# Performance work log

Measured on AMD Instinct MI355X. Metric: run time of the kernel, lower is better.

## Reference

```python
import jax, jax.numpy as jnp
import numpy as np

C = 4096
IN_DIM = 256
OUT_DIM = 64
H = 4
NEG_SLOPE = 0.2


def setup_inputs() -> dict:
    key = jax.random.key(0)
    k_x, k_adj, k_w, k_as, k_ad = jax.random.split(key, 5)
    x = jax.random.normal(k_x, (C, IN_DIM), dtype=jnp.float32)
    adj = jax.random.randint(k_adj, (C, C), 0, 2, dtype=jnp.int32)
    # xavier_uniform for Linear(in, out*H): bound = sqrt(6/(fan_in+fan_out))
    bw = float(np.sqrt(6.0 / (IN_DIM + OUT_DIM * H)))
    W = jax.random.uniform(k_w, (IN_DIM, OUT_DIM * H), minval=-bw, maxval=bw, dtype=jnp.float32)
    ba = float(np.sqrt(6.0 / (H + OUT_DIM)))
    a_src = jax.random.uniform(k_as, (H, OUT_DIM), minval=-ba, maxval=ba, dtype=jnp.float32)
    a_dst = jax.random.uniform(k_ad, (H, OUT_DIM), minval=-ba, maxval=ba, dtype=jnp.float32)
    return {"x": x, "adj": adj, "W": W, "a_src": a_src, "a_dst": a_dst}


def reference(x, adj, W, a_src, a_dst):
    # h: [C, H, D] -> h_heads: [H, C, D]
    h = (x @ W).reshape(C, H, OUT_DIM)
    h_heads = jnp.transpose(h, (1, 0, 2))
    # per-node additive attention logits: [H, C]
    alpha_src = jnp.einsum('hcd,hd->hc', h_heads, a_src)
    alpha_dst = jnp.einsum('hcd,hd->hc', h_heads, a_dst)
    # broadcast scores e: [H, C, C]
    e = alpha_src[:, :, None] + alpha_dst[:, None, :]
    e = jnp.where(e >= 0, e, NEG_SLOPE * e)  # LeakyReLU
    e = jnp.where(adj[None, :, :] == 0, -jnp.inf, e)
    attn = jax.nn.softmax(e, axis=-1)  # [H, C, C]
    out = jnp.einsum('hcj,hjd->hcd', attn, h_heads)  # [H, C, D]
    return jnp.transpose(out, (1, 0, 2)).reshape(C, H * OUT_DIM)
```

## Files before the change

kernel.cpp:

```cpp
#include <hip/hip_runtime.h>
#include <math.h>

#define CN 4096
#define KDIM 256
#define ND 256
#define NH 4
#define DD 64
#define NEG 0.2f
#define L2E 1.44269504f

typedef __attribute__((ext_vector_type(8))) short short8;
typedef __attribute__((ext_vector_type(4))) float floatx4;

union S8I4 { int i[4]; short8 s; };

__device__ inline unsigned bfbits_rne(float f) {
  unsigned u = __float_as_uint(f);
  u += 0x7fffu + ((u >> 16) & 1u);
  return u >> 16;
}
__device__ inline float bf2f(unsigned hi) { return __uint_as_float(hi << 16); }

__device__ inline int pack2_trunc(float a, float b) {
  return (int)__builtin_amdgcn_perm(__float_as_uint(b), __float_as_uint(a), 0x07060302u);
}

#define GLDS(gp, lp, sz)                                                        \
  __builtin_amdgcn_global_load_lds(                                             \
      (const __attribute__((address_space(1))) void*)(gp),                      \
      (__attribute__((address_space(3))) void*)(lp), (sz), 0, 0)

__global__ __launch_bounds__(256) void k_wcvt(const float* __restrict__ W,
                                              unsigned short* __restrict__ WT_hi,
                                              unsigned short* __restrict__ WT_lo) {
  const int t = threadIdx.x;
  const int c = blockIdx.x * 4 + (t >> 6);
  const int k0 = (t & 63) * 4;
  unsigned h[4], l[4];
#pragma unroll
  for (int j = 0; j < 4; ++j) {
    const float w = W[(size_t)(k0 + j) * ND + c];
    h[j] = bfbits_rne(w);
    l[j] = bfbits_rne(w - bf2f(h[j]));
  }
  uint2 vh, vl;
  vh.x = h[0] | (h[1] << 16); vh.y = h[2] | (h[3] << 16);
  vl.x = l[0] | (l[1] << 16); vl.y = l[2] | (l[3] << 16);
  *(uint2*)&WT_hi[(size_t)c * KDIM + k0] = vh;
  *(uint2*)&WT_lo[(size_t)c * KDIM + k0] = vl;
}

__global__ __launch_bounds__(256) void k_pre(const int* __restrict__ adj,
                                             unsigned char* __restrict__ mbits8,
                                             const float* __restrict__ x,
                                             const unsigned short* __restrict__ WT_hi,
                                             const unsigned short* __restrict__ WT_lo,
                                             const float* __restrict__ a_src,
                                             const float* __restrict__ a_dst,
                                             unsigned short* __restrict__ hT,
                                             float2* __restrict__ Erow,
                                             float2* __restrict__ Ecol) {
  const int bx = blockIdx.x;
  const int t = threadIdx.x;
  if (bx >= 256) {
    const int w = t >> 6, lane = t & 63;
    const int row = (bx - 256) * 4 + w;
    const int4* __restrict__ src = (const int4*)(adj + (size_t)row * CN);
    unsigned char* __restrict__ dst = mbits8 + (size_t)row * 512;
#pragma unroll
    for (int it = 0; it < 8; ++it) {
      const int4 v0 = src[it * 128 + lane * 2];
      const int4 v1 = src[it * 128 + lane * 2 + 1];
      const unsigned b = (unsigned)(v0.x != 0)        | ((unsigned)(v0.y != 0) << 1) |
                         ((unsigned)(v0.z != 0) << 2) | ((unsigned)(v0.w != 0) << 3) |
                         ((unsigned)(v1.x != 0) << 4) | ((unsigned)(v1.y != 0) << 5) |
                         ((unsigned)(v1.z != 0) << 6) | ((unsigned)(v1.w != 0) << 7);
      dst[it * 64 + lane] = (unsigned char)b;
    }
    return;
  }
  const int lane = t & 63, ww = t >> 6;
  const int n = lane & 15, q = lane >> 4;
  const int head = bx >> 6;
  const int c0 = head * DD;
  const int i0 = (bx & 63) * 64 + ww * 16;
  const float* xr = x + (size_t)(i0 + n) * KDIM + q * 8;
  floatx4 acc[4] = {};
#pragma unroll 2
  for (int k0 = 0; k0 < KDIM; k0 += 32) {
    const float4 xa = *(const float4*)(xr + k0);
    const float4 xb = *(const float4*)(xr + k0 + 4);
    const float xs[8] = {xa.x, xa.y, xa.z, xa.w, xb.x, xb.y, xb.z, xb.w};
    S8I4 Ah, Al;
#pragma unroll
    for (int e = 0; e < 4; ++e) {
      const unsigned h0 = bfbits_rne(xs[2 * e]), h1 = bfbits_rne(xs[2 * e + 1]);
      const float r0 = xs[2 * e] - bf2f(h0), r1 = xs[2 * e + 1] - bf2f(h1);
      Ah.i[e] = (int)(h0 | (h1 << 16));
      Al.i[e] = (int)(bfbits_rne(r0) | (bfbits_rne(r1) << 16));
    }
#pragma unroll
    for (int tt = 0; tt < 4; ++tt) {
      const size_t boff = (size_t)(c0 + tt * 16 + n) * KDIM + k0 + q * 8;
      const short8 Bh = *(const short8*)(WT_hi + boff);
      const short8 Bl = *(const short8*)(WT_lo + boff);
      acc[tt] = __builtin_amdgcn_mfma_f32_16x16x32_bf16(Ah.s, Bh, acc[tt], 0, 0, 0);
      acc[tt] = __builtin_amdgcn_mfma_f32_16x16x32_bf16(Al.s, Bh, acc[tt], 0, 0, 0);
      acc[tt] = __builtin_amdgcn_mfma_f32_16x16x32_bf16(Ah.s, Bl, acc[tt], 0, 0, 0);
    }
  }
  unsigned short* hTb = hT + (size_t)head * DD * CN;
#pragma unroll
  for (int tt = 0; tt < 4; ++tt)
#pragma unroll
    for (int r = 0; r < 4; r += 2) {
      const unsigned d = bfbits_rne(acc[tt][r]) | (bfbits_rne(acc[tt][r + 1]) << 16);
      *(unsigned*)(hTb + (size_t)(tt * 16 + n) * CN + i0 + q * 4 + r) = d;
    }
  float ps[4] = {}, pd[4] = {};
#pragma unroll
  for (int tt = 0; tt < 4; ++tt) {
    const float as = a_src[head * DD + tt * 16 + n];
    const float ad = a_dst[head * DD + tt * 16 + n];
#pragma unroll
    for (int r = 0; r < 4; ++r) {
      ps[r] += acc[tt][r] * as;
      pd[r] += acc[tt][r] * ad;
    }
  }
#pragma unroll
  for (int off = 1; off < 16; off <<= 1)
#pragma unroll
    for (int r = 0; r < 4; ++r) {
      ps[r] += __shfl_xor(ps[r], off);
      pd[r] += __shfl_xor(pd[r], off);
    }
  if (n == 0) {
#pragma unroll
    for (int r = 0; r < 4; ++r) {
      const int i = i0 + q * 4 + r;
      const float as_ = ps[r] * L2E, ad_ = pd[r] * L2E;
      Erow[head * CN + i] = make_float2(__builtin_amdgcn_exp2f(as_),
                                        __builtin_amdgcn_exp2f(NEG * as_));
      Ecol[head * CN + i] = make_float2(__builtin_amdgcn_exp2f(ad_),
                                        __builtin_amdgcn_exp2f(NEG * ad_));
    }
  }
}

__global__ __launch_bounds__(512, 4) void k_attn(const unsigned short* __restrict__ hT,
                                                 const unsigned* __restrict__ mbits32,
                                                 const float2* __restrict__ Erow,
                                                 const float2* __restrict__ Ecol,
                                                 float* __restrict__ out) {
  __shared__ __align__(16) char smem[8 * 2 * 4608];
  const int t = threadIdx.x;
  const int lane = t & 63, ww = t >> 6;
  const int n = lane & 15, q = lane >> 4;
  const int head = blockIdx.y;
  const int i0 = blockIdx.x * 32;
  const unsigned short* __restrict__ hTb = hT + (size_t)head * DD * CN;
  const float* __restrict__ ecf = (const float*)(Ecol + (size_t)head * CN);
  const int jbase = ww * 512;

  const float2 es0 = Erow[head * CN + i0 + n];
  const float2 es1 = Erow[head * CN + i0 + 16 + n];

  const unsigned hoff =
      (unsigned)(lane >> 2) * CN + (((lane & 3) ^ ((lane >> 3) & 3)) * 8);
  const unsigned mrow = (unsigned)(i0 + (lane & 31)) * 128;
  char* const wbase = smem + ww * 2 * 4608;

  short8 ONES;
#pragma unroll
  for (int u = 0; u < 8; ++u) ONES[u] = (short)0x3F80;

  floatx4 acc[2][4] = {};
  floatx4 accz[2] = {};

  auto ISSUE = [&](int b, int j0) {
    char* base = wbase + b * 4608;
#pragma unroll
    for (int g = 0; g < 4; ++g)
      GLDS(hTb + (size_t)(g * 16) * CN + hoff + j0, base + g * 1024, 16);
    GLDS(mbits32 + mrow + (j0 >> 5), base + 4096, 4);
    GLDS(ecf + j0 * 2 + lane, base + 4352, 4);
  };

  ISSUE(0, jbase);
  for (int c = 0; c < 16; ++c) {
    if (c < 15) {
      ISSUE((c + 1) & 1, jbase + (c + 1) * 32);
      asm volatile("s_waitcnt vmcnt(6)" ::: "memory");
    } else {
      asm volatile("s_waitcnt vmcnt(0)" ::: "memory");
    }
    const char* base = wbase + (c & 1) * 4608;
    short8 B[4];
#pragma unroll
    for (int tt = 0; tt < 4; ++tt)
      B[tt] = *(const short8*)(base + (tt * 16 + n) * 64 +
                               ((q ^ ((n >> 1) & 3)) << 4));
    const unsigned m0 = *(const unsigned*)(base + 4096 + n * 4);
    const unsigned m1 = *(const unsigned*)(base + 4096 + (16 + n) * 4);
    const unsigned mb0 = (m0 >> (q * 8)) & 255u;
    const unsigned mb1 = (m1 >> (q * 8)) & 255u;
    const float4* adl4 = (const float4*)(base + 4352);
    S8I4 A[2];
#pragma unroll
    for (int g = 0; g < 4; ++g) {
      const float4 v = adl4[q * 4 + g];
#pragma unroll
      for (int rg = 0; rg < 2; ++rg) {
        const float2 es = rg ? es1 : es0;
        const unsigned mb = rg ? mb1 : mb0;
        float w0 = fmaxf(es.x * v.x, es.y * v.y);
        float w1 = fmaxf(es.x * v.z, es.y * v.w);
        w0 = ((mb >> (2 * g)) & 1u) ? w0 : 0.0f;
        w1 = ((mb >> (2 * g + 1)) & 1u) ? w1 : 0.0f;
        A[rg].i[g] = pack2_trunc(w0, w1);
      }
    }
#pragma unroll
    for (int rg = 0; rg < 2; ++rg) {
      accz[rg] = __builtin_amdgcn_mfma_f32_16x16x32_bf16(A[rg].s, ONES, accz[rg], 0, 0, 0);
#pragma unroll
      for (int tt = 0; tt < 4; ++tt)
        acc[rg][tt] =
            __builtin_amdgcn_mfma_f32_16x16x32_bf16(A[rg].s, B[tt], acc[rg][tt], 0, 0, 0);
    }
  }

  __syncthreads();
  float* red = (float*)smem;
  if (ww > 0) {
    float* rb = red + (ww - 1) * 2560;
#pragma unroll
    for (int rg = 0; rg < 2; ++rg) {
#pragma unroll
      for (int tt = 0; tt < 4; ++tt)
#pragma unroll
        for (int r = 0; r < 4; ++r)
          rb[(rg * 20 + tt * 4 + r) * 64 + lane] = acc[rg][tt][r];
#pragma unroll
      for (int r = 0; r < 4; ++r) rb[(rg * 20 + 16 + r) * 64 + lane] = accz[rg][r];
    }
  }
  __syncthreads();
  if (ww == 0) {
#pragma unroll
    for (int s = 0; s < 7; ++s) {
      const float* rb = red + s * 2560;
#pragma unroll
      for (int rg = 0; rg < 2; ++rg) {
#pragma unroll
        for (int tt = 0; tt < 4; ++tt)
#pragma unroll
          for (int r = 0; r < 4; ++r)
            acc[rg][tt][r] += rb[(rg * 20 + tt * 4 + r) * 64 + lane];
#pragma unroll
        for (int r = 0; r < 4; ++r) accz[rg][r] += rb[(rg * 20 + 16 + r) * 64 + lane];
      }
    }
#pragma unroll
    for (int rg = 0; rg < 2; ++rg)
#pragma unroll
      for (int r = 0; r < 4; ++r) {
        const float iz = 1.0f / accz[rg][r];
        float* orow = out + (size_t)(i0 + rg * 16 + q * 4 + r) * ND + head * DD + n;
#pragma unroll
        for (int tt = 0; tt < 4; ++tt) orow[tt * 16] = acc[rg][tt][r] * iz;
      }
  }
}

extern "C" void kernel_launch(void* const* d_in, const int* in_sizes, int n_in,
                              void* d_out, int out_size, void* d_ws, size_t ws_size,
                              hipStream_t stream) {
  const float* x = (const float*)d_in[0];
  const int* adj = (const int*)d_in[1];
  const float* W = (const float*)d_in[2];
  const float* a_src = (const float*)d_in[3];
  const float* a_dst = (const float*)d_in[4];
  float* out = (float*)d_out;

  unsigned short* hT = (unsigned short*)d_ws;
  float2* Erow = (float2*)(hT + (size_t)NH * DD * CN);
  float2* Ecol = Erow + (size_t)NH * CN;
  unsigned short* WT_hi = (unsigned short*)(Ecol + (size_t)NH * CN);
  unsigned short* WT_lo = WT_hi + (size_t)ND * KDIM;
  unsigned char* mbits8 = (unsigned char*)(WT_lo + (size_t)ND * KDIM);

  k_wcvt<<<dim3(ND / 4), 256, 0, stream>>>(W, WT_hi, WT_lo);
  k_pre<<<dim3(256 + CN / 4), 256, 0, stream>>>(adj, mbits8, x, WT_hi, WT_lo,
                                                a_src, a_dst, hT, Erow, Ecol);
  k_attn<<<dim3(CN / 32, NH), 512, 0, stream>>>(hT, (const unsigned*)mbits8,
                                                Erow, Ecol, out);
}
```

Baseline: 141.7 us.

## Split attention over key quarters with shared hT tiles and separate finalize kernel

Restructures k_attn so each 256-thread block handles 64 query rows against one quarter of the keys. Its four waves share a block-wide, double-buffered LDS tile of hT and the column exponentials, and results are written as partial numerators and denominators. A new k_fin kernel sums the four partials and normalizes. The column exponentials are stored as packed bf16 pairs to halve their traffic. The aim is to replace the per-wave private staging and intra-block reduction with cross-wave reuse of hT and more independent blocks. The cost is an extra kernel launch, a round trip of roughly 16 MB of partial results through global memory, and bf16 rounding of the exponentials.

```diff
diff --git a/kernel.cpp b/kernel.cpp
--- a/kernel.cpp
+++ b/kernel.cpp
@@ -59,7 +59,7 @@
                                              const float* __restrict__ a_dst,
                                              unsigned short* __restrict__ hT,
                                              float2* __restrict__ Erow,
-                                             float2* __restrict__ Ecol) {
+                                             unsigned* __restrict__ Ecol_bf) {
   const int bx = blockIdx.x;
   const int t = threadIdx.x;
   if (bx >= 256) {
@@ -142,136 +142,116 @@
       const float as_ = ps[r] * L2E, ad_ = pd[r] * L2E;
       Erow[head * CN + i] = make_float2(__builtin_amdgcn_exp2f(as_),
                                         __builtin_amdgcn_exp2f(NEG * as_));
-      Ecol[head * CN + i] = make_float2(__builtin_amdgcn_exp2f(ad_),
-                                        __builtin_amdgcn_exp2f(NEG * ad_));
-    }
-  }
-}
-
-__global__ __launch_bounds__(512, 4) void k_attn(const unsigned short* __restrict__ hT,
-                                                 const unsigned* __restrict__ mbits32,
+      Ecol_bf[head * CN + i] = bfbits_rne(__builtin_amdgcn_exp2f(ad_)) |
+                               (bfbits_rne(__builtin_amdgcn_exp2f(NEG * ad_)) << 16);
+    }
+  }
+}
+
+__global__ __launch_bounds__(256, 4) void k_attn(const unsigned short* __restrict__ hT,
+                                                 const unsigned char* __restrict__ mbits8,
                                                  const float2* __restrict__ Erow,
-                                                 const float2* __restrict__ Ecol,
-                                                 float* __restrict__ out) {
-  __shared__ __align__(16) char smem[8 * 2 * 4608];
+                                                 const unsigned* __restrict__ Ecol_bf,
+                                                 float* __restrict__ P,
+                                                 float* __restrict__ Zb) {
+  __shared__ __align__(16) char smem[2][8448];
   const int t = threadIdx.x;
   const int lane = t & 63, ww = t >> 6;
   const int n = lane & 15, q = lane >> 4;
   const int head = blockIdx.y;
-  const int i0 = blockIdx.x * 32;
+  const int jq = blockIdx.z;
+  const int i0 = blockIdx.x * 64;
+  const int jbase = jq * 1024;
   const unsigned short* __restrict__ hTb = hT + (size_t)head * DD * CN;
-  const float* __restrict__ ecf = (const float*)(Ecol + (size_t)head * CN);
-  const int jbase = ww * 512;
-
-  const float2 es0 = Erow[head * CN + i0 + n];
-  const float2 es1 = Erow[head * CN + i0 + 16 + n];
-
-  const unsigned hoff =
-      (unsigned)(lane >> 2) * CN + (((lane & 3) ^ ((lane >> 3) & 3)) * 8);
-  const unsigned mrow = (unsigned)(i0 + (lane & 31)) * 128;
-  char* const wbase = smem + ww * 2 * 4608;
+  const unsigned* __restrict__ ecb = Ecol_bf + (size_t)head * CN;
+  const int myrow = i0 + ww * 16 + n;
+  const float2 es = Erow[head * CN + myrow];
+  const unsigned char* __restrict__ mrow = mbits8 + (size_t)myrow * 512;
+
+  const unsigned hsw = (unsigned)(lane >> 3) * CN + (((lane & 7) ^ (lane >> 3)) * 8);
 
   short8 ONES;
 #pragma unroll
   for (int u = 0; u < 8; ++u) ONES[u] = (short)0x3F80;
 
-  floatx4 acc[2][4] = {};
-  floatx4 accz[2] = {};
-
-  auto ISSUE = [&](int b, int j0) {
-    char* base = wbase + b * 4608;
-#pragma unroll
-    for (int g = 0; g < 4; ++g)
-      GLDS(hTb + (size_t)(g * 16) * CN + hoff + j0, base + g * 1024, 16);
-    GLDS(mbits32 + mrow + (j0 >> 5), base + 4096, 4);
-    GLDS(ecf + j0 * 2 + lane, base + 4352, 4);
+  floatx4 acc[4] = {};
+  floatx4 accz = {};
+
+  auto STAGE = [&](int b, int j0) {
+    char* base = smem[b];
+    GLDS(hTb + (size_t)(ww * 16) * CN + hsw + j0, base + ww * 2048, 16);
+    GLDS(hTb + (size_t)(ww * 16 + 8) * CN + hsw + j0, base + ww * 2048 + 1024, 16);
+    if (ww == 0) GLDS(ecb + j0 + lane, base + 8192, 4);
   };
 
-  ISSUE(0, jbase);
+  unsigned m0 = mrow[(jbase >> 3) + q];
+  unsigned m1 = mrow[(jbase >> 3) + q + 4];
+  STAGE(0, jbase);
   for (int c = 0; c < 16; ++c) {
+    const int j0 = jbase + c * 64;
+    __syncthreads();
+    unsigned m0n = 0, m1n = 0;
     if (c < 15) {
-      ISSUE((c + 1) & 1, jbase + (c + 1) * 32);
-      asm volatile("s_waitcnt vmcnt(6)" ::: "memory");
-    } else {
-      asm volatile("s_waitcnt vmcnt(0)" ::: "memory");
-    }
-    const char* base = wbase + (c & 1) * 4608;
-    short8 B[4];
-#pragma unroll
-    for (int tt = 0; tt < 4; ++tt)
-      B[tt] = *(const short8*)(base + (tt * 16 + n) * 64 +
-                               ((q ^ ((n >> 1) & 3)) << 4));
-    const unsigned m0 = *(const unsigned*)(base + 4096 + n * 4);
-    const unsigned m1 = *(const unsigned*)(base + 4096 + (16 + n) * 4);
-    const unsigned mb0 = (m0 >> (q * 8)) & 255u;
-    const unsigned mb1 = (m1 >> (q * 8)) & 255u;
-    const float4* adl4 = (const float4*)(base + 4352);
-    S8I4 A[2];
-#pragma unroll
-    for (int g = 0; g < 4; ++g) {
-      const float4 v = adl4[q * 4 + g];
-#pragma unroll
-      for (int rg = 0; rg < 2; ++rg) {
-        const float2 es = rg ? es1 : es0;
-        const unsigned mb = rg ? mb1 : mb0;
-        float w0 = fmaxf(es.x * v.x, es.y * v.y);
-        float w1 = fmaxf(es.x * v.z, es.y * v.w);
-        w0 = ((mb >> (2 * g)) & 1u) ? w0 : 0.0f;
-        w1 = ((mb >> (2 * g + 1)) & 1u) ? w1 : 0.0f;
-        A[rg].i[g] = pack2_trunc(w0, w1);
+      STAGE((c + 1) & 1, j0 + 64);
+      m0n = mrow[((j0 + 64) >> 3) + q];
+      m1n = mrow[((j0 + 64) >> 3) + q + 4];
+    }
+    const char* base = smem[c & 1];
+#pragma unroll
+    for (int kf = 0; kf < 2; ++kf) {
+      short8 B[4];
+#pragma unroll
+      for (int tt = 0; tt < 4; ++tt)
+        B[tt] = *(const short8*)(base + (tt * 16 + n) * 128 +
+                                 (((kf * 4 + q) ^ (n & 7)) << 4));
+      const uint4 e0 = *(const uint4*)(base + 8192 + (kf * 32 + q * 8) * 4);
+      const uint4 e1 = *(const uint4*)(base + 8192 + (kf * 32 + q * 8) * 4 + 16);
+      const unsigned ev[8] = {e0.x, e0.y, e0.z, e0.w, e1.x, e1.y, e1.z, e1.w};
+      const unsigned mb = kf ? m1 : m0;
+      float fv[8];
+#pragma unroll
+      for (int e = 0; e < 8; ++e) {
+        const float Ed = __uint_as_float(ev[e] << 16);
+        const float Ed2 = __uint_as_float(ev[e] & 0xffff0000u);
+        const float w = fmaxf(es.x * Ed, es.y * Ed2);
+        fv[e] = ((mb >> e) & 1u) ? w : 0.0f;
       }
-    }
-#pragma unroll
-    for (int rg = 0; rg < 2; ++rg) {
-      accz[rg] = __builtin_amdgcn_mfma_f32_16x16x32_bf16(A[rg].s, ONES, accz[rg], 0, 0, 0);
+      S8I4 A;
+#pragma unroll
+      for (int e = 0; e < 4; ++e) A.i[e] = pack2_trunc(fv[2 * e], fv[2 * e + 1]);
+      accz = __builtin_amdgcn_mfma_f32_16x16x32_bf16(A.s, ONES, accz, 0, 0, 0);
 #pragma unroll
       for (int tt = 0; tt < 4; ++tt)
-        acc[rg][tt] =
-            __builtin_amdgcn_mfma_f32_16x16x32_bf16(A[rg].s, B[tt], acc[rg][tt], 0, 0, 0);
-    }
-  }
-
-  __syncthreads();
-  float* red = (float*)smem;
-  if (ww > 0) {
-    float* rb = red + (ww - 1) * 2560;
-#pragma unroll
-    for (int rg = 0; rg < 2; ++rg) {
-#pragma unroll
-      for (int tt = 0; tt < 4; ++tt)
-#pragma unroll
-        for (int r = 0; r < 4; ++r)
-          rb[(rg * 20 + tt * 4 + r) * 64 + lane] = acc[rg][tt][r];
-#pragma unroll
-      for (int r = 0; r < 4; ++r) rb[(rg * 20 + 16 + r) * 64 + lane] = accz[rg][r];
-    }
-  }
-  __syncthreads();
-  if (ww == 0) {
-#pragma unroll
-    for (int s = 0; s < 7; ++s) {
-      const float* rb = red + s * 2560;
-#pragma unroll
-      for (int rg = 0; rg < 2; ++rg) {
-#pragma unroll
-        for (int tt = 0; tt < 4; ++tt)
-#pragma unroll
-          for (int r = 0; r < 4; ++r)
-            acc[rg][tt][r] += rb[(rg * 20 + tt * 4 + r) * 64 + lane];
-#pragma unroll
-        for (int r = 0; r < 4; ++r) accz[rg][r] += rb[(rg * 20 + 16 + r) * 64 + lane];
-      }
-    }
-#pragma unroll
-    for (int rg = 0; rg < 2; ++rg)
-#pragma unroll
-      for (int r = 0; r < 4; ++r) {
-        const float iz = 1.0f / accz[rg][r];
-        float* orow = out + (size_t)(i0 + rg * 16 + q * 4 + r) * ND + head * DD + n;
-#pragma unroll
-        for (int tt = 0; tt < 4; ++tt) orow[tt * 16] = acc[rg][tt][r] * iz;
-      }
-  }
+        acc[tt] = __builtin_amdgcn_mfma_f32_16x16x32_bf16(A.s, B[tt], acc[tt], 0, 0, 0);
+    }
+    m0 = m0n; m1 = m1n;
+    __syncthreads();
+  }
+
+  float* Pp = P + ((size_t)(jq * NH + head) * CN + i0) * DD;
+  float* Zp = Zb + (size_t)(jq * NH + head) * CN + i0;
+#pragma unroll
+  for (int r = 0; r < 4; ++r) {
+    const int rl = ww * 16 + q * 4 + r;
+#pragma unroll
+    for (int tt = 0; tt < 4; ++tt) Pp[(size_t)rl * DD + tt * 16 + n] = acc[tt][r];
+    if (n == 0) Zp[rl] = accz[r];
+  }
+}
+
+__global__ __launch_bounds__(256) void k_fin(const float* __restrict__ P,
+                                             const float* __restrict__ Zb,
+                                             float* __restrict__ out) {
+  const int i = blockIdx.x;
+  const int t = threadIdx.x;
+  const int head = t >> 6, d = t & 63;
+  float num = 0.f, z = 0.f;
+#pragma unroll
+  for (int jqq = 0; jqq < 4; ++jqq) {
+    num += P[((size_t)(jqq * NH + head) * CN + i) * DD + d];
+    z += Zb[(size_t)(jqq * NH + head) * CN + i];
+  }
+  out[(size_t)i * ND + head * DD + d] = num / z;
 }
 
 extern "C" void kernel_launch(void* const* d_in, const int* in_sizes, int n_in,
@@ -286,14 +266,16 @@
 
   unsigned short* hT = (unsigned short*)d_ws;
   float2* Erow = (float2*)(hT + (size_t)NH * DD * CN);
-  float2* Ecol = Erow + (size_t)NH * CN;
-  unsigned short* WT_hi = (unsigned short*)(Ecol + (size_t)NH * CN);
+  unsigned* Ecol_bf = (unsigned*)(Erow + (size_t)NH * CN);
+  unsigned short* WT_hi = (unsigned short*)(Ecol_bf + (size_t)NH * CN);
   unsigned short* WT_lo = WT_hi + (size_t)ND * KDIM;
   unsigned char* mbits8 = (unsigned char*)(WT_lo + (size_t)ND * KDIM);
+  float* P = (float*)(mbits8 + (size_t)CN * 512);
+  float* Zb = P + (size_t)4 * NH * CN * DD;
 
   k_wcvt<<<dim3(ND / 4), 256, 0, stream>>>(W, WT_hi, WT_lo);
   k_pre<<<dim3(256 + CN / 4), 256, 0, stream>>>(adj, mbits8, x, WT_hi, WT_lo,
-                                                a_src, a_dst, hT, Erow, Ecol);
-  k_attn<<<dim3(CN / 32, NH), 512, 0, stream>>>(hT, (const unsigned*)mbits8,
-                                                Erow, Ecol, out);
-}
+                                                a_src, a_dst, hT, Erow, Ecol_bf);
+  k_attn<<<dim3(CN / 64, NH, 4), 256, 0, stream>>>(hT, mbits8, Erow, Ecol_bf, P, Zb);
+  k_fin<<<dim3(CN), 256, 0, stream>>>(P, Zb, out);
+}
```

Result: slower. 148.3 us (+4.7%).

## Fuse W bf16 split conversion into k_pre via shared memory staging

Applied to the files above, without the earlier changes.

Removes the separate k_wcvt launch and instead has each GEMM block convert its 64-column W slice into hi/lo bf16 in padded LDS, then read B fragments from LDS. It also software-prefetches the next x chunk into registers. This eliminates one kernel launch and a global round trip for WT. The cost is that every one of the 256 GEMM blocks redundantly converts its W slice with strided global reads, and the 66KB of LDS per block limits occupancy. That LDS is also allocated by the mask-packing blocks.

```diff
diff --git a/kernel.cpp b/kernel.cpp
--- a/kernel.cpp
+++ b/kernel.cpp
@@ -30,36 +30,17 @@
       (const __attribute__((address_space(1))) void*)(gp),                      \
       (__attribute__((address_space(3))) void*)(lp), (sz), 0, 0)
 
-__global__ __launch_bounds__(256) void k_wcvt(const float* __restrict__ W,
-                                              unsigned short* __restrict__ WT_hi,
-                                              unsigned short* __restrict__ WT_lo) {
-  const int t = threadIdx.x;
-  const int c = blockIdx.x * 4 + (t >> 6);
-  const int k0 = (t & 63) * 4;
-  unsigned h[4], l[4];
-#pragma unroll
-  for (int j = 0; j < 4; ++j) {
-    const float w = W[(size_t)(k0 + j) * ND + c];
-    h[j] = bfbits_rne(w);
-    l[j] = bfbits_rne(w - bf2f(h[j]));
-  }
-  uint2 vh, vl;
-  vh.x = h[0] | (h[1] << 16); vh.y = h[2] | (h[3] << 16);
-  vl.x = l[0] | (l[1] << 16); vl.y = l[2] | (l[3] << 16);
-  *(uint2*)&WT_hi[(size_t)c * KDIM + k0] = vh;
-  *(uint2*)&WT_lo[(size_t)c * KDIM + k0] = vl;
-}
-
-__global__ __launch_bounds__(256) void k_pre(const int* __restrict__ adj,
-                                             unsigned char* __restrict__ mbits8,
-                                             const float* __restrict__ x,
-                                             const unsigned short* __restrict__ WT_hi,
-                                             const unsigned short* __restrict__ WT_lo,
-                                             const float* __restrict__ a_src,
-                                             const float* __restrict__ a_dst,
-                                             unsigned short* __restrict__ hT,
-                                             float2* __restrict__ Erow,
-                                             float2* __restrict__ Ecol) {
+__global__ __launch_bounds__(256, 2) void k_pre(const int* __restrict__ adj,
+                                                unsigned char* __restrict__ mbits8,
+                                                const float* __restrict__ x,
+                                                const float* __restrict__ W,
+                                                const float* __restrict__ a_src,
+                                                const float* __restrict__ a_dst,
+                                                unsigned short* __restrict__ hT,
+                                                float2* __restrict__ Erow,
+                                                float2* __restrict__ Ecol) {
+  __shared__ __align__(16) unsigned short Whi_s[64 * 264];
+  __shared__ __align__(16) unsigned short Wlo_s[64 * 264];
   const int bx = blockIdx.x;
   const int t = threadIdx.x;
   if (bx >= 256) {
@@ -84,13 +65,30 @@
   const int head = bx >> 6;
   const int c0 = head * DD;
   const int i0 = (bx & 63) * 64 + ww * 16;
+  {
+    const int c = t & 63, kb = t >> 6;
+    const float* Wc = W + c0 + c;
+#pragma unroll 8
+    for (int p = 0; p < 64; ++p) {
+      const int k = p * 4 + kb;
+      const float w = Wc[(size_t)k * ND];
+      const unsigned hi = bfbits_rne(w);
+      const unsigned lo = bfbits_rne(w - bf2f(hi));
+      Whi_s[c * 264 + k] = (unsigned short)hi;
+      Wlo_s[c * 264 + k] = (unsigned short)lo;
+    }
+  }
   const float* xr = x + (size_t)(i0 + n) * KDIM + q * 8;
+  float4 xa = *(const float4*)(xr);
+  float4 xb = *(const float4*)(xr + 4);
+  __syncthreads();
   floatx4 acc[4] = {};
-#pragma unroll 2
   for (int k0 = 0; k0 < KDIM; k0 += 32) {
-    const float4 xa = *(const float4*)(xr + k0);
-    const float4 xb = *(const float4*)(xr + k0 + 4);
     const float xs[8] = {xa.x, xa.y, xa.z, xa.w, xb.x, xb.y, xb.z, xb.w};
+    if (k0 + 32 < KDIM) {
+      xa = *(const float4*)(xr + k0 + 32);
+      xb = *(const float4*)(xr + k0 + 36);
+    }
     S8I4 Ah, Al;
 #pragma unroll
     for (int e = 0; e < 4; ++e) {
@@ -101,9 +99,9 @@
     }
 #pragma unroll
     for (int tt = 0; tt < 4; ++tt) {
-      const size_t boff = (size_t)(c0 + tt * 16 + n) * KDIM + k0 + q * 8;
-      const short8 Bh = *(const short8*)(WT_hi + boff);
-      const short8 Bl = *(const short8*)(WT_lo + boff);
+      const int boff = (tt * 16 + n) * 264 + k0 + q * 8;
+      const short8 Bh = *(const short8*)&Whi_s[boff];
+      const short8 Bl = *(const short8*)&Wlo_s[boff];
       acc[tt] = __builtin_amdgcn_mfma_f32_16x16x32_bf16(Ah.s, Bh, acc[tt], 0, 0, 0);
       acc[tt] = __builtin_amdgcn_mfma_f32_16x16x32_bf16(Al.s, Bh, acc[tt], 0, 0, 0);
       acc[tt] = __builtin_amdgcn_mfma_f32_16x16x32_bf16(Ah.s, Bl, acc[tt], 0, 0, 0);
@@ -287,12 +285,9 @@
   unsigned short* hT = (unsigned short*)d_ws;
   float2* Erow = (float2*)(hT + (size_t)NH * DD * CN);
   float2* Ecol = Erow + (size_t)NH * CN;
-  unsigned short* WT_hi = (unsigned short*)(Ecol + (size_t)NH * CN);
-  unsigned short* WT_lo = WT_hi + (size_t)ND * KDIM;
-  unsigned char* mbits8 = (unsigned char*)(WT_lo + (size_t)ND * KDIM);
-
-  k_wcvt<<<dim3(ND / 4), 256, 0, stream>>>(W, WT_hi, WT_lo);
-  k_pre<<<dim3(256 + CN / 4), 256, 0, stream>>>(adj, mbits8, x, WT_hi, WT_lo,
+  unsigned char* mbits8 = (unsigned char*)(Ecol + (size_t)NH * CN);
+
+  k_pre<<<dim3(256 + CN / 4), 256, 0, stream>>>(adj, mbits8, x, W,
                                                 a_src, a_dst, hT, Erow, Ecol);
   k_attn<<<dim3(CN / 32, NH), 512, 0, stream>>>(hT, (const unsigned*)mbits8,
                                                 Erow, Ecol, out);
```

Result: faster. 136.0 us (-4.0%).
